# Kernel optimization log

Measured on AMD Instinct MI355X. Metric: run time of the kernel, lower is better.

## Reference

```python
import jax, jax.numpy as jnp
import numpy as np

N_NODES = 100000
N_EDGES = 1600000
D_IN = 128
D_HID = 128
D_EMB = 128
D_OUT = 16


def _glorot(key, shape):
    fan_in, fan_out = shape
    lim = (6.0 / (fan_in + fan_out)) ** 0.5
    return jax.random.uniform(key, shape, jnp.float32, -lim, lim)


def setup_inputs() -> dict:
    key = jax.random.key(0)
    ks = jax.random.split(key, 12)
    x = jax.random.normal(ks[0], (N_NODES, D_IN), jnp.float32)
    edge_index = jax.random.randint(ks[1], (2, N_EDGES), 0, N_NODES, jnp.int32)
    return {
        "x": x,
        "edge_index": edge_index,
        # SAGEConv layer 0: neighbor weight, self(root) weight, bias
        "Wn0": _glorot(ks[2], (D_IN, D_HID)),
        "Ws0": _glorot(ks[3], (D_IN, D_HID)),
        "b0": jnp.zeros((D_HID,), jnp.float32),
        # SAGEConv layer 1
        "Wn1": _glorot(ks[4], (D_HID, D_HID)),
        "Ws1": _glorot(ks[5], (D_HID, D_HID)),
        "b1": jnp.zeros((D_HID,), jnp.float32),
        # SAGEConv layer 2 (to embedding dim)
        "Wn2": _glorot(ks[6], (D_HID, D_EMB)),
        "Ws2": _glorot(ks[7], (D_HID, D_EMB)),
        "b2": jnp.zeros((D_EMB,), jnp.float32),
        # final fc
        "Wfc": _glorot(ks[8], (D_EMB, D_OUT)),
        "bfc": jnp.zeros((D_OUT,), jnp.float32),
    }


def _sage_conv(x, src, dst, deg_inv, Wn, Ws, b):
    # mean-aggregate source features at destination nodes, then transform.
    agg = jax.ops.segment_sum(x[src], dst, num_segments=N_NODES)  # [N, d]
    mean = agg * deg_inv[:, None]
    return mean @ Wn + x @ Ws + b


def reference(x, edge_index, Wn0, Ws0, b0, Wn1, Ws1, b1, Wn2, Ws2, b2, Wfc, bfc):
    src, dst = edge_index[0], edge_index[1]
    deg = jax.ops.segment_sum(jnp.ones((src.shape[0],), x.dtype), dst,
                              num_segments=N_NODES)
    deg_inv = 1.0 / jnp.maximum(deg, 1.0)

    h = _sage_conv(x, src, dst, deg_inv, Wn0, Ws0, b0)
    h = jax.nn.relu(h)  # dropout omitted (eval mode / deterministic reference)
    h = _sage_conv(h, src, dst, deg_inv, Wn1, Ws1, b1)
    h = jax.nn.relu(h)
    emb = _sage_conv(h, src, dst, deg_inv, Wn2, Ws2, b2)
    y = emb @ Wfc + bfc
    return emb, jax.nn.log_softmax(y, axis=1)
```

## Files before the change

kernel.cpp:

```cpp
#include <hip/hip_runtime.h>
#include <hip/hip_fp16.h>

#define NN 100000
#define NE 1600000
#define DD 128
#define CAP 48
#define FRAG_ELEMS 16384

#define NRNG 8
#define RNODES 12500
#define EPT 8
#define FILL_T (NE / EPT)
#define FILL_BPR ((FILL_T + 255) / 256)

typedef __attribute__((ext_vector_type(8))) _Float16 half8;
typedef __attribute__((ext_vector_type(4))) float f32x4;

__global__ void k_xcast(const float* __restrict__ x, _Float16* __restrict__ xh,
                        int* __restrict__ cnt) {
    int t = blockIdx.x * 256 + threadIdx.x;
    if (t < NN) cnt[t] = 0;
    const float* p = x + (size_t)t * 8;
    float4 v0 = *(const float4*)p;
    float4 v1 = *(const float4*)(p + 4);
    half8 o = { (_Float16)v0.x, (_Float16)v0.y, (_Float16)v0.z, (_Float16)v0.w,
                (_Float16)v1.x, (_Float16)v1.y, (_Float16)v1.z, (_Float16)v1.w };
    *(half8*)(xh + (size_t)t * 8) = o;
}

__global__ __launch_bounds__(256) void k_fill(const int* __restrict__ src,
                                              const int* __restrict__ dst,
                                              int* __restrict__ cnt,
                                              int* __restrict__ bkt) {
    int rng = blockIdx.x & (NRNG - 1);
    int t = (blockIdx.x >> 3) * 256 + threadIdx.x;
    if (t >= FILL_T) return;
    int lo = rng * RNODES;
    const int4* d4 = (const int4*)dst;
    const int4* s4 = (const int4*)src;
    int4 d0 = d4[t * 2];
    int4 d1 = d4[t * 2 + 1];
    int4 s0 = s4[t * 2];
    int4 s1 = s4[t * 2 + 1];
    int dd[8] = { d0.x, d0.y, d0.z, d0.w, d1.x, d1.y, d1.z, d1.w };
    int ss[8] = { s0.x, s0.y, s0.z, s0.w, s1.x, s1.y, s1.z, s1.w };
#pragma unroll
    for (int k = 0; k < 8; ++k) {
        int d = dd[k];
        unsigned rel = (unsigned)(d - lo);
        if (rel < (unsigned)RNODES) {
            int p = atomicAdd(&cnt[d], 1);
            if (p < CAP) bkt[(size_t)d * CAP + p] = ss[k];
        }
    }
}

__global__ __launch_bounds__(256) void k_wprep(const float* __restrict__ W0,
                                               const float* __restrict__ W1,
                                               const float* __restrict__ W2,
                                               const float* __restrict__ W3,
                                               const float* __restrict__ W4,
                                               const float* __restrict__ W5,
                                               _Float16* __restrict__ out) {
    int mat = blockIdx.x >> 6;
    int e = (blockIdx.x & 63) * 256 + threadIdx.x;
    const float* W = (mat == 0) ? W0 : (mat == 1) ? W1 : (mat == 2) ? W2
                   : (mat == 3) ? W3 : (mat == 4) ? W4 : W5;
    int j = e & 7;
    int lane = (e >> 3) & 63;
    int ct = (e >> 9) & 7;
    int kt = e >> 12;
    int k = kt * 32 + (lane >> 4) * 8 + j;
    int n = ct * 16 + (lane & 15);
    float v = W[k * 128 + n];
    _Float16 hi = (_Float16)v;
    _Float16 lo = (_Float16)(v - (float)hi);
    _Float16* mb = out + (size_t)mat * 2 * FRAG_ELEMS;
    mb[e] = hi;
    mb[FRAG_ELEMS + e] = lo;
}

__global__ __launch_bounds__(256) void k_agg(const _Float16* __restrict__ h,
                                             const int* __restrict__ cnt,
                                             const int* __restrict__ bkt,
                                             _Float16* __restrict__ mean) {
    int node = blockIdx.x * 4 + (threadIdx.x >> 6);
    if (node >= NN) return;
    int lane = threadIdx.x & 63;
    int q = lane >> 4;
    int col = (lane & 15) * 8;
    int deg = cnt[node];
    int n = deg > CAP ? CAP : deg;
    const int* b = bkt + (size_t)node * CAP;
    float a[8] = {};
    int i = 0;
    for (; i + 16 <= n; i += 16) {
        int s0 = b[i + q];
        int s1 = b[i + 4 + q];
        int s2 = b[i + 8 + q];
        int s3 = b[i + 12 + q];
        half8 v0 = *(const half8*)(h + (size_t)s0 * DD + col);
        half8 v1 = *(const half8*)(h + (size_t)s1 * DD + col);
        half8 v2 = *(const half8*)(h + (size_t)s2 * DD + col);
        half8 v3 = *(const half8*)(h + (size_t)s3 * DD + col);
#pragma unroll
        for (int j = 0; j < 8; ++j)
            a[j] += ((float)v0[j] + (float)v1[j]) + ((float)v2[j] + (float)v3[j]);
    }
    if (i + 8 <= n) {
        int s0 = b[i + q];
        int s1 = b[i + 4 + q];
        half8 v0 = *(const half8*)(h + (size_t)s0 * DD + col);
        half8 v1 = *(const half8*)(h + (size_t)s1 * DD + col);
#pragma unroll
        for (int j = 0; j < 8; ++j) a[j] += (float)v0[j] + (float)v1[j];
        i += 8;
    }
    if (i + 4 <= n) {
        int s0 = b[i + q];
        half8 v0 = *(const half8*)(h + (size_t)s0 * DD + col);
#pragma unroll
        for (int j = 0; j < 8; ++j) a[j] += (float)v0[j];
        i += 4;
    }
    if (i + q < n) {
        int s = b[i + q];
        half8 v = *(const half8*)(h + (size_t)s * DD + col);
#pragma unroll
        for (int j = 0; j < 8; ++j) a[j] += (float)v[j];
    }
#pragma unroll
    for (int j = 0; j < 8; ++j) {
        a[j] += __shfl_xor(a[j], 16);
        a[j] += __shfl_xor(a[j], 32);
    }
    if (q == 0) {
        float di = 1.0f / (float)(deg > 1 ? deg : 1);
        half8 o;
#pragma unroll
        for (int j = 0; j < 8; ++j) o[j] = (_Float16)(a[j] * di);
        *(half8*)(mean + (size_t)node * DD + col) = o;
    }
}

__global__ __launch_bounds__(256) void k_gemm(
    const _Float16* __restrict__ meanp, const _Float16* __restrict__ hin,
    const _Float16* __restrict__ wf,
    const float* __restrict__ bias,
    _Float16* __restrict__ outh, float* __restrict__ outf) {

    __shared__ _Float16 sw[2][4096];

    int t = threadIdx.x;
    int wave = t >> 6;
    int lane = t & 63;
    int m16 = lane & 15;
    int kg = lane >> 4;
    int rowA = blockIdx.x * 64 + wave * 16 + m16;
    if (rowA >= NN) rowA = NN - 1;

    half8 afrag[2][4];
    {
        const _Float16* Am = meanp + (size_t)rowA * DD + kg * 8;
        const _Float16* Ah = hin  + (size_t)rowA * DD + kg * 8;
#pragma unroll
        for (int kt = 0; kt < 4; ++kt) {
            afrag[0][kt] = *(const half8*)(Am + kt * 32);
            afrag[1][kt] = *(const half8*)(Ah + kt * 32);
        }
    }

    half8 ph0, ph1, pl0, pl1;
    {
        const half8* gh = (const half8*)(wf);
        const half8* gl = (const half8*)(wf + FRAG_ELEMS);
        ph0 = gh[t]; ph1 = gh[t + 256];
        pl0 = gl[t]; pl1 = gl[t + 256];
    }

    f32x4 acc[8] = {};

#pragma unroll
    for (int idx = 0; idx < 8; ++idx) {
        int s = idx >> 2;
        int kt = idx & 3;
        __syncthreads();
        {
            half8* dsth = (half8*)sw[0];
            half8* dstl = (half8*)sw[1];
            dsth[t]       = ph0;
            dsth[t + 256] = ph1;
            dstl[t]       = pl0;
            dstl[t + 256] = pl1;
        }
        if (idx < 7) {
            int s2 = (idx + 1) >> 2;
            int kt2 = (idx + 1) & 3;
            const half8* gh = (const half8*)(wf + s2 * 2 * FRAG_ELEMS + kt2 * 4096);
            const half8* gl = (const half8*)(wf + s2 * 2 * FRAG_ELEMS + FRAG_ELEMS + kt2 * 4096);
            ph0 = gh[t]; ph1 = gh[t + 256];
            pl0 = gl[t]; pl1 = gl[t + 256];
        }
        __syncthreads();
        half8 a = afrag[s][kt];
#pragma unroll
        for (int ct = 0; ct < 8; ++ct) {
            half8 bh = *(const half8*)(sw[0] + (ct * 64 + lane) * 8);
            half8 bl = *(const half8*)(sw[1] + (ct * 64 + lane) * 8);
            acc[ct] = __builtin_amdgcn_mfma_f32_16x16x32_f16(a, bh, acc[ct], 0, 0, 0);
            acc[ct] = __builtin_amdgcn_mfma_f32_16x16x32_f16(a, bl, acc[ct], 0, 0, 0);
        }
    }

    int rbase = blockIdx.x * 64 + wave * 16 + kg * 4;
    if (outh) {
#pragma unroll
        for (int ct = 0; ct < 8; ++ct) {
            int col = ct * 16 + m16;
            float bv = bias[col];
#pragma unroll
            for (int i = 0; i < 4; ++i) {
                int r = rbase + i;
                if (r < NN)
                    outh[(size_t)r * DD + col] = (_Float16)fmaxf(acc[ct][i] + bv, 0.0f);
            }
        }
    } else {
#pragma unroll
        for (int ct = 0; ct < 8; ++ct) {
            int col = ct * 16 + m16;
            float bv = bias[col];
#pragma unroll
            for (int i = 0; i < 4; ++i) {
                int r = rbase + i;
                if (r < NN)
                    outf[(size_t)r * DD + col] = acc[ct][i] + bv;
            }
        }
    }
}

__global__ __launch_bounds__(256) void k_fc(const float* __restrict__ emb,
                                            const float* __restrict__ Wfc,
                                            const float* __restrict__ bfc,
                                            float* __restrict__ out) {
    __shared__ float se[16 * 128];
    __shared__ float swt[128 * 16];
    int t = threadIdx.x;
    int nb = blockIdx.x * 16;
    int idx = t * 8;
    *(float4*)(se + idx)      = *(const float4*)(emb + (size_t)nb * 128 + idx);
    *(float4*)(se + idx + 4)  = *(const float4*)(emb + (size_t)nb * 128 + idx + 4);
    *(float4*)(swt + idx)     = *(const float4*)(Wfc + idx);
    *(float4*)(swt + idx + 4) = *(const float4*)(Wfc + idx + 4);
    __syncthreads();

    int nl = t >> 4;
    int o = t & 15;
    float acc = bfc[o];
    const float* er = se + nl * 128;
#pragma unroll 8
    for (int k = 0; k < 128; ++k)
        acc += er[k] * swt[k * 16 + o];

    float m = acc;
#pragma unroll
    for (int d = 1; d < 16; d <<= 1) m = fmaxf(m, __shfl_xor(m, d, 16));
    float e = expf(acc - m);
    float ssum = e;
#pragma unroll
    for (int d = 1; d < 16; d <<= 1) ssum += __shfl_xor(ssum, d, 16);
    out[(size_t)(nb + nl) * 16 + o] = (acc - m) - logf(ssum);
}

extern "C" void kernel_launch(void* const* d_in, const int* in_sizes, int n_in,
                              void* d_out, int out_size, void* d_ws, size_t ws_size,
                              hipStream_t stream) {
    const float* x   = (const float*)d_in[0];
    const int*   ei  = (const int*)d_in[1];
    const float* Wn0 = (const float*)d_in[2];
    const float* Ws0 = (const float*)d_in[3];
    const float* b0  = (const float*)d_in[4];
    const float* Wn1 = (const float*)d_in[5];
    const float* Ws1 = (const float*)d_in[6];
    const float* b1  = (const float*)d_in[7];
    const float* Wn2 = (const float*)d_in[8];
    const float* Ws2 = (const float*)d_in[9];
    const float* b2  = (const float*)d_in[10];
    const float* Wfc = (const float*)d_in[11];
    const float* bfc = (const float*)d_in[12];

    const int* src = ei;
    const int* dst = ei + NE;

    float* emb_out = (float*)d_out;
    float* lsm_out = emb_out + (size_t)NN * 128;

    char* ws = (char*)d_ws;
    _Float16* xh    = (_Float16*)(ws);
    _Float16* hA    = (_Float16*)(ws + 25600000);
    _Float16* hB    = (_Float16*)(ws + 51200000);
    _Float16* mean  = (_Float16*)(ws + 76800000);
    int*      cnt   = (int*)     (ws + 102400000);
    int*      bkt   = (int*)     (ws + 102800000);
    _Float16* wfrag = (_Float16*)(ws + 122000000);

    k_xcast<<<(NN * DD / 8) / 256, 256, 0, stream>>>(x, xh, cnt);
    k_wprep<<<384, 256, 0, stream>>>(Wn0, Ws0, Wn1, Ws1, Wn2, Ws2, wfrag);
    k_fill<<<NRNG * FILL_BPR, 256, 0, stream>>>(src, dst, cnt, bkt);

    const int agg_blocks  = (NN + 3) / 4;
    const int gemm_blocks = (NN + 63) / 64;
    _Float16* wf0 = wfrag;
    _Float16* wf1 = wfrag + 4 * FRAG_ELEMS;
    _Float16* wf2 = wfrag + 8 * FRAG_ELEMS;

    k_agg<<<agg_blocks, 256, 0, stream>>>(xh, cnt, bkt, mean);
    k_gemm<<<gemm_blocks, 256, 0, stream>>>(mean, xh, wf0, b0, hA, nullptr);

    k_agg<<<agg_blocks, 256, 0, stream>>>(hA, cnt, bkt, mean);
    k_gemm<<<gemm_blocks, 256, 0, stream>>>(mean, hA, wf1, b1, hB, nullptr);

    k_agg<<<agg_blocks, 256, 0, stream>>>(hB, cnt, bkt, mean);
    k_gemm<<<gemm_blocks, 256, 0, stream>>>(mean, hB, wf2, b2, nullptr, emb_out);

    k_fc<<<NN / 16, 256, 0, stream>>>(emb_out, Wfc, bfc, lsm_out);
}
```

Measured before the change: 488.5 us.

## Merge prep kernels into one launch and fuse final FC log-softmax into last GEMM

The x-cast, weight-prep and edge-bucket fill kernels are combined into a single launch that dispatches on block index, with the count zeroing moved to a memset. The final fc plus log_softmax is computed in the epilogue of the last GEMM from register-held embeddings, using Wfc staged in shared memory and butterfly shuffles across the 16 column lanes. This removes two launches and the re-read of the fp32 embedding matrix. In exchange the GEMM epilogue has more register pressure and shuffle work, and the fill atomics now share a launch with the cast traffic.

```diff
diff --git a/kernel.cpp b/kernel.cpp
--- a/kernel.cpp
+++ b/kernel.cpp
@@ -12,72 +12,74 @@
 #define EPT 8
 #define FILL_T (NE / EPT)
 #define FILL_BPR ((FILL_T + 255) / 256)
+#define FILL_B (NRNG * FILL_BPR)
+#define XCAST_B ((NN * DD / 8) / 256)
+#define PREP_B (FILL_B + XCAST_B + 384)
 
 typedef __attribute__((ext_vector_type(8))) _Float16 half8;
 typedef __attribute__((ext_vector_type(4))) float f32x4;
 
-__global__ void k_xcast(const float* __restrict__ x, _Float16* __restrict__ xh,
-                        int* __restrict__ cnt) {
-    int t = blockIdx.x * 256 + threadIdx.x;
-    if (t < NN) cnt[t] = 0;
-    const float* p = x + (size_t)t * 8;
-    float4 v0 = *(const float4*)p;
-    float4 v1 = *(const float4*)(p + 4);
-    half8 o = { (_Float16)v0.x, (_Float16)v0.y, (_Float16)v0.z, (_Float16)v0.w,
-                (_Float16)v1.x, (_Float16)v1.y, (_Float16)v1.z, (_Float16)v1.w };
-    *(half8*)(xh + (size_t)t * 8) = o;
-}
-
-__global__ __launch_bounds__(256) void k_fill(const int* __restrict__ src,
-                                              const int* __restrict__ dst,
-                                              int* __restrict__ cnt,
-                                              int* __restrict__ bkt) {
-    int rng = blockIdx.x & (NRNG - 1);
-    int t = (blockIdx.x >> 3) * 256 + threadIdx.x;
-    if (t >= FILL_T) return;
-    int lo = rng * RNODES;
-    const int4* d4 = (const int4*)dst;
-    const int4* s4 = (const int4*)src;
-    int4 d0 = d4[t * 2];
-    int4 d1 = d4[t * 2 + 1];
-    int4 s0 = s4[t * 2];
-    int4 s1 = s4[t * 2 + 1];
-    int dd[8] = { d0.x, d0.y, d0.z, d0.w, d1.x, d1.y, d1.z, d1.w };
-    int ss[8] = { s0.x, s0.y, s0.z, s0.w, s1.x, s1.y, s1.z, s1.w };
-#pragma unroll
-    for (int k = 0; k < 8; ++k) {
-        int d = dd[k];
-        unsigned rel = (unsigned)(d - lo);
-        if (rel < (unsigned)RNODES) {
-            int p = atomicAdd(&cnt[d], 1);
-            if (p < CAP) bkt[(size_t)d * CAP + p] = ss[k];
-        }
-    }
-}
-
-__global__ __launch_bounds__(256) void k_wprep(const float* __restrict__ W0,
-                                               const float* __restrict__ W1,
-                                               const float* __restrict__ W2,
-                                               const float* __restrict__ W3,
-                                               const float* __restrict__ W4,
-                                               const float* __restrict__ W5,
-                                               _Float16* __restrict__ out) {
-    int mat = blockIdx.x >> 6;
-    int e = (blockIdx.x & 63) * 256 + threadIdx.x;
-    const float* W = (mat == 0) ? W0 : (mat == 1) ? W1 : (mat == 2) ? W2
-                   : (mat == 3) ? W3 : (mat == 4) ? W4 : W5;
-    int j = e & 7;
-    int lane = (e >> 3) & 63;
-    int ct = (e >> 9) & 7;
-    int kt = e >> 12;
-    int k = kt * 32 + (lane >> 4) * 8 + j;
-    int n = ct * 16 + (lane & 15);
-    float v = W[k * 128 + n];
-    _Float16 hi = (_Float16)v;
-    _Float16 lo = (_Float16)(v - (float)hi);
-    _Float16* mb = out + (size_t)mat * 2 * FRAG_ELEMS;
-    mb[e] = hi;
-    mb[FRAG_ELEMS + e] = lo;
+__global__ __launch_bounds__(256) void k_prep(
+    const int* __restrict__ src, const int* __restrict__ dst,
+    int* __restrict__ cnt, int* __restrict__ bkt,
+    const float* __restrict__ x, _Float16* __restrict__ xh,
+    const float* __restrict__ W0, const float* __restrict__ W1,
+    const float* __restrict__ W2, const float* __restrict__ W3,
+    const float* __restrict__ W4, const float* __restrict__ W5,
+    _Float16* __restrict__ wfrag) {
+
+    int b = blockIdx.x;
+    int tid = threadIdx.x;
+
+    if (b < FILL_B) {
+        int rng = b & (NRNG - 1);
+        int t = (b >> 3) * 256 + tid;
+        if (t >= FILL_T) return;
+        int lo = rng * RNODES;
+        const int4* d4 = (const int4*)dst;
+        const int4* s4 = (const int4*)src;
+        int4 d0 = d4[t * 2];
+        int4 d1 = d4[t * 2 + 1];
+        int4 s0 = s4[t * 2];
+        int4 s1 = s4[t * 2 + 1];
+        int dd[8] = { d0.x, d0.y, d0.z, d0.w, d1.x, d1.y, d1.z, d1.w };
+        int ss[8] = { s0.x, s0.y, s0.z, s0.w, s1.x, s1.y, s1.z, s1.w };
+#pragma unroll
+        for (int k = 0; k < 8; ++k) {
+            int d = dd[k];
+            unsigned rel = (unsigned)(d - lo);
+            if (rel < (unsigned)RNODES) {
+                int p = atomicAdd(&cnt[d], 1);
+                if (p < CAP) bkt[(size_t)d * CAP + p] = ss[k];
+            }
+        }
+    } else if (b < FILL_B + XCAST_B) {
+        int t = (b - FILL_B) * 256 + tid;
+        const float* p = x + (size_t)t * 8;
+        float4 v0 = *(const float4*)p;
+        float4 v1 = *(const float4*)(p + 4);
+        half8 o = { (_Float16)v0.x, (_Float16)v0.y, (_Float16)v0.z, (_Float16)v0.w,
+                    (_Float16)v1.x, (_Float16)v1.y, (_Float16)v1.z, (_Float16)v1.w };
+        *(half8*)(xh + (size_t)t * 8) = o;
+    } else {
+        int wb = b - FILL_B - XCAST_B;
+        int mat = wb >> 6;
+        int e = (wb & 63) * 256 + tid;
+        const float* W = (mat == 0) ? W0 : (mat == 1) ? W1 : (mat == 2) ? W2
+                       : (mat == 3) ? W3 : (mat == 4) ? W4 : W5;
+        int j = e & 7;
+        int lane = (e >> 3) & 63;
+        int ct = (e >> 9) & 7;
+        int kt = e >> 12;
+        int k = kt * 32 + (lane >> 4) * 8 + j;
+        int n = ct * 16 + (lane & 15);
+        float v = W[k * 128 + n];
+        _Float16 hi = (_Float16)v;
+        _Float16 lo = (_Float16)(v - (float)hi);
+        _Float16* mb = wfrag + (size_t)mat * 2 * FRAG_ELEMS;
+        mb[e] = hi;
+        mb[FRAG_ELEMS + e] = lo;
+    }
 }
 
 __global__ __launch_bounds__(256) void k_agg(const _Float16* __restrict__ h,
@@ -147,7 +149,9 @@
     const _Float16* __restrict__ meanp, const _Float16* __restrict__ hin,
     const _Float16* __restrict__ wf,
     const float* __restrict__ bias,
-    _Float16* __restrict__ outh, float* __restrict__ outf) {
+    _Float16* __restrict__ outh, float* __restrict__ outf,
+    const float* __restrict__ Wfc, const float* __restrict__ bfc,
+    float* __restrict__ lsm) {
 
     __shared__ _Float16 sw[2][4096];
 
@@ -226,51 +230,64 @@
             }
         }
     } else {
+        float embv[8][4];
 #pragma unroll
         for (int ct = 0; ct < 8; ++ct) {
             int col = ct * 16 + m16;
             float bv = bias[col];
 #pragma unroll
             for (int i = 0; i < 4; ++i) {
+                embv[ct][i] = acc[ct][i] + bv;
                 int r = rbase + i;
                 if (r < NN)
-                    outf[(size_t)r * DD + col] = acc[ct][i] + bv;
-            }
-        }
-    }
-}
-
-__global__ __launch_bounds__(256) void k_fc(const float* __restrict__ emb,
-                                            const float* __restrict__ Wfc,
-                                            const float* __restrict__ bfc,
-                                            float* __restrict__ out) {
-    __shared__ float se[16 * 128];
-    __shared__ float swt[128 * 16];
-    int t = threadIdx.x;
-    int nb = blockIdx.x * 16;
-    int idx = t * 8;
-    *(float4*)(se + idx)      = *(const float4*)(emb + (size_t)nb * 128 + idx);
-    *(float4*)(se + idx + 4)  = *(const float4*)(emb + (size_t)nb * 128 + idx + 4);
-    *(float4*)(swt + idx)     = *(const float4*)(Wfc + idx);
-    *(float4*)(swt + idx + 4) = *(const float4*)(Wfc + idx + 4);
-    __syncthreads();
-
-    int nl = t >> 4;
-    int o = t & 15;
-    float acc = bfc[o];
-    const float* er = se + nl * 128;
-#pragma unroll 8
-    for (int k = 0; k < 128; ++k)
-        acc += er[k] * swt[k * 16 + o];
-
-    float m = acc;
-#pragma unroll
-    for (int d = 1; d < 16; d <<= 1) m = fmaxf(m, __shfl_xor(m, d, 16));
-    float e = expf(acc - m);
-    float ssum = e;
-#pragma unroll
-    for (int d = 1; d < 16; d <<= 1) ssum += __shfl_xor(ssum, d, 16);
-    out[(size_t)(nb + nl) * 16 + o] = (acc - m) - logf(ssum);
+                    outf[(size_t)r * DD + col] = embv[ct][i];
+            }
+        }
+        __syncthreads();
+        float* swf = (float*)sw;
+        *(float4*)(swf + t * 8)     = *(const float4*)(Wfc + t * 8);
+        *(float4*)(swf + t * 8 + 4) = *(const float4*)(Wfc + t * 8 + 4);
+        __syncthreads();
+#pragma unroll
+        for (int i = 0; i < 4; ++i) {
+            float p[16];
+#pragma unroll
+            for (int o = 0; o < 16; ++o) p[o] = 0.0f;
+#pragma unroll
+            for (int ct = 0; ct < 8; ++ct) {
+                const float* wr = swf + (ct * 16 + m16) * 16;
+                float4 w0 = *(const float4*)(wr);
+                float4 w1 = *(const float4*)(wr + 4);
+                float4 w2 = *(const float4*)(wr + 8);
+                float4 w3 = *(const float4*)(wr + 12);
+                float e = embv[ct][i];
+                p[0]  += e * w0.x; p[1]  += e * w0.y; p[2]  += e * w0.z; p[3]  += e * w0.w;
+                p[4]  += e * w1.x; p[5]  += e * w1.y; p[6]  += e * w1.z; p[7]  += e * w1.w;
+                p[8]  += e * w2.x; p[9]  += e * w2.y; p[10] += e * w2.z; p[11] += e * w2.w;
+                p[12] += e * w3.x; p[13] += e * w3.y; p[14] += e * w3.z; p[15] += e * w3.w;
+            }
+#pragma unroll
+            for (int d = 1; d < 16; d <<= 1) {
+#pragma unroll
+                for (int o = 0; o < 16; ++o) p[o] += __shfl_xor(p[o], d);
+            }
+#pragma unroll
+            for (int o = 0; o < 16; ++o) p[o] += bfc[o];
+            float mx = p[0];
+#pragma unroll
+            for (int o = 1; o < 16; ++o) mx = fmaxf(mx, p[o]);
+            float se = 0.0f;
+#pragma unroll
+            for (int o = 0; o < 16; ++o) se += expf(p[o] - mx);
+            float lse = mx + logf(se);
+            float val = p[0];
+#pragma unroll
+            for (int o = 1; o < 16; ++o) val = (m16 == o) ? p[o] : val;
+            int r = rbase + i;
+            if (r < NN)
+                lsm[(size_t)r * 16 + m16] = val - lse;
+        }
+    }
 }
 
 extern "C" void kernel_launch(void* const* d_in, const int* in_sizes, int n_in,
@@ -305,9 +322,9 @@
     int*      bkt   = (int*)     (ws + 102800000);
     _Float16* wfrag = (_Float16*)(ws + 122000000);
 
-    k_xcast<<<(NN * DD / 8) / 256, 256, 0, stream>>>(x, xh, cnt);
-    k_wprep<<<384, 256, 0, stream>>>(Wn0, Ws0, Wn1, Ws1, Wn2, Ws2, wfrag);
-    k_fill<<<NRNG * FILL_BPR, 256, 0, stream>>>(src, dst, cnt, bkt);
+    hipMemsetAsync(cnt, 0, NN * sizeof(int), stream);
+    k_prep<<<PREP_B, 256, 0, stream>>>(src, dst, cnt, bkt, x, xh,
+                                       Wn0, Ws0, Wn1, Ws1, Wn2, Ws2, wfrag);
 
     const int agg_blocks  = (NN + 3) / 4;
     const int gemm_blocks = (NN + 63) / 64;
@@ -316,13 +333,14 @@
     _Float16* wf2 = wfrag + 8 * FRAG_ELEMS;
 
     k_agg<<<agg_blocks, 256, 0, stream>>>(xh, cnt, bkt, mean);
-    k_gemm<<<gemm_blocks, 256, 0, stream>>>(mean, xh, wf0, b0, hA, nullptr);
+    k_gemm<<<gemm_blocks, 256, 0, stream>>>(mean, xh, wf0, b0, hA, nullptr,
+                                            nullptr, nullptr, nullptr);
 
     k_agg<<<agg_blocks, 256, 0, stream>>>(hA, cnt, bkt, mean);
-    k_gemm<<<gemm_blocks, 256, 0, stream>>>(mean, hA, wf1, b1, hB, nullptr);
+    k_gemm<<<gemm_blocks, 256, 0, stream>>>(mean, hA, wf1, b1, hB, nullptr,
+                                            nullptr, nullptr, nullptr);
 
     k_agg<<<agg_blocks, 256, 0, stream>>>(hB, cnt, bkt, mean);
-    k_gemm<<<gemm_blocks, 256, 0, stream>>>(mean, hB, wf2, b2, nullptr, emb_out);
-
-    k_fc<<<NN / 16, 256, 0, stream>>>(emb_out, Wfc, bfc, lsm_out);
+    k_gemm<<<gemm_blocks, 256, 0, stream>>>(mean, hB, wf2, b2, nullptr, emb_out,
+                                            Wfc, bfc, lsm_out);
 }
```

After: 500.3 us. +2.4%, slower.
